# Performance work log

Measured on AMD Instinct MI355X. Metric: run time of the kernel, lower is better.

The kernel has to match this reference:

```python
import jax, jax.numpy as jnp
import numpy as np

K = 16  # number of neighbors (module init arg)

def setup_inputs() -> dict:
    key = jax.random.key(0)
    M, D, N = 65536, 16, 64
    x = jax.random.normal(key, (M, D), dtype=jnp.float32)
    # equal-length segments: each point set has M // N points
    segs = jnp.full((N,), M // N, dtype=jnp.int64)
    return {"x": x, "segs": segs}

def reference(x, segs):
    # Segmented kNN graph. Segments are equal-length (static shapes for jit),
    # so the per-segment pairwise distance + top-k becomes a batched op.
    B = segs.shape[0]
    M, D = x.shape
    L = M // B  # points per segment
    pts = x.reshape(B, L, D)
    # squared euclidean distances within each segment: (B, L, L)
    sq = jnp.sum(pts * pts, axis=-1)
    d2 = sq[:, :, None] + sq[:, None, :] - 2.0 * jnp.einsum('bld,bmd->blm', pts, pts)
    # k smallest distances per point (includes self, as in DGL's knn_graph)
    _, idx = jax.lax.top_k(-d2, K)  # idx: (B, L, K), local indices within segment
    offsets = (jnp.arange(B, dtype=idx.dtype) * L)[:, None, None]
    src = (idx + offsets).reshape(-1)                      # neighbor -> global node id
    dst = (jnp.arange(L, dtype=idx.dtype)[None, :, None] + offsets)  # (B, L, 1)
    dst = jnp.broadcast_to(dst, (B, L, K)).reshape(-1)
    # edges point from k-nearest neighbors (predecessors) to each node
    return src, dst
```

## Files before the change

kernel.cpp:

```cpp
#include <hip/hip_runtime.h>
#include <stdint.h>


#define L_SEG 1024
#define M_PTS 65536

typedef __fp16 fp16x2 __attribute__((ext_vector_type(2)));
typedef __fp16 fp16x4 __attribute__((ext_vector_type(4)));
typedef float  f32x4  __attribute__((ext_vector_type(4)));

__device__ __forceinline__ uint32_t umn(uint32_t a, uint32_t b) { return a < b ? a : b; }
__device__ __forceinline__ uint32_t umx(uint32_t a, uint32_t b) { return a > b ? a : b; }

#define CE(arr, i, p) { uint32_t lo = umn(arr[i], arr[p]); uint32_t hi = umx(arr[i], arr[p]); arr[i] = lo; arr[p] = hi; }

__device__ __forceinline__ void clean16(uint32_t* A) {
    #pragma unroll
    for (int j = 8; j > 0; j >>= 1) {
        #pragma unroll
        for (int i = 0; i < 16; ++i) {
            int p = i ^ j;
            if (p > i) CE(A, i, p);
        }
    }
}

__device__ __forceinline__ void sort16(uint32_t* B) {
    #pragma unroll
    for (int p = 1; p < 16; p <<= 1) {
        #pragma unroll
        for (int k = p; k >= 1; k >>= 1) {
            #pragma unroll
            for (int j = (k & (p - 1)); j + k < 16; j += 2 * k) {
                #pragma unroll
                for (int i = 0; i <= ((k - 1 < 15 - j - k) ? k - 1 : 15 - j - k); ++i) {
                    if ((i + j) / (2 * p) == (i + j + k) / (2 * p)) CE(B, i + j, i + j + k);
                }
            }
        }
    }
}

__device__ __forceinline__ void keep16(uint32_t* A, const uint32_t* S) {
    #pragma unroll
    for (int i = 0; i < 16; ++i) A[i] = umn(A[i], S[15 - i]);
    clean16(A);
}

__device__ __forceinline__ void mergeg(uint32_t* A) {
    #pragma unroll
    for (int m = 16; m <= 32; m <<= 1) {
        uint32_t P[16];
        #pragma unroll
        for (int i = 0; i < 16; ++i) P[i] = (uint32_t)__shfl_xor((int)A[15 - i], m, 64);
        #pragma unroll
        for (int i = 0; i < 16; ++i) A[i] = umn(A[i], P[i]);
        clean16(A);
    }
}

__device__ __forceinline__ uint32_t sel4(const uint32_t* A, int g, int v) {
    uint32_t t01 = (g & 1) ? A[4 + v]  : A[v];
    uint32_t t23 = (g & 1) ? A[12 + v] : A[8 + v];
    return (g & 2) ? t23 : t01;
}

__device__ __forceinline__ void batch16(const __fp16* ap, const float* sqp,
                                        fp16x4 bfrag, int it, int g, uint32_t* P) {
    #pragma unroll
    for (int t = 0; t < 16; ++t) {
        const int cb = it * 256 + t * 16;
        fp16x4 af = *(const fp16x4*)(ap + (size_t)cb * 16);
        f32x4  sq = *(const f32x4*)(sqp + cb);
        f32x4 acc = __builtin_amdgcn_mfma_f32_16x16x16f16(af, bfrag, sq, 0, 0, 0);
        float m = fminf(fminf(fminf(acc[0], acc[1]), acc[2]), acc[3]);
        P[t] = (__float_as_uint(m) & 0xFFFFFF00u) | (uint32_t)(it * 64 + t * 4) | (uint32_t)g;
    }
}

__global__ __launch_bounds__(1024, 1) void knn_v17_kernel(const float* __restrict__ x,
                                                          int* __restrict__ out) {
    __shared__ __attribute__((aligned(16))) __fp16 sc[L_SEG * 16];
    __shared__ __attribute__((aligned(16))) float  ssq[L_SEG];

    const int tid  = threadIdx.x;
    const int b    = blockIdx.x;
    const int seg  = b >> 2;
    const int qgrp = (b & 3) << 8;
    const float* xseg = x + (size_t)seg * (L_SEG * 16);
    const f32x4* gx4  = (const f32x4*)xseg;

    {
        fp16x4* scv = (fp16x4*)sc;
        const int widx = (tid & ~3) + ((tid & 3) ^ ((tid >> 4) & 3));
        #pragma unroll
        for (int i = 0; i < 4; ++i) {
            f32x4 v = gx4[tid + 1024 * i];
            union { fp16x2 h2[2]; fp16x4 h4; } u;
            u.h2[0] = __builtin_amdgcn_cvt_pkrtz(-2.0f * v[0], -2.0f * v[1]);
            u.h2[1] = __builtin_amdgcn_cvt_pkrtz(-2.0f * v[2], -2.0f * v[3]);
            scv[widx + 1024 * i] = u.h4;
            float p = v[0] * v[0];
            p = __builtin_fmaf(v[1], v[1], p);
            p = __builtin_fmaf(v[2], v[2], p);
            p = __builtin_fmaf(v[3], v[3], p);
            p += __shfl_xor(p, 1, 64);
            p += __shfl_xor(p, 2, 64);
            if ((tid & 3) == 0) ssq[(tid >> 2) + 256 * i] = p + 128.0f;
        }
    }
    __syncthreads();

    const int lane = tid & 63;
    const int w    = tid >> 6;
    const int g    = lane >> 4;
    const int col  = lane & 15;
    const int qrow = qgrp + w * 16 + col;
    const int gsw  = g ^ ((col >> 2) & 3);

    const fp16x4 mh = {(__fp16)-0.5f, (__fp16)-0.5f, (__fp16)-0.5f, (__fp16)-0.5f};
    fp16x4 bfrag;
    {
        fp16x4 raw = *(const fp16x4*)(sc + (size_t)qrow * 16 + gsw * 4);
        bfrag = raw * mh;
    }

    const __fp16* ap  = sc + (size_t)col * 16 + gsw * 4;
    const float*  sqp = ssq + g * 4;

    uint32_t P0[16], P1[16], P2[16], P3[16];
    batch16(ap, sqp, bfrag, 0, g, P0);
    batch16(ap, sqp, bfrag, 1, g, P1);
    batch16(ap, sqp, bfrag, 2, g, P2);
    batch16(ap, sqp, bfrag, 3, g, P3);
    sort16(P0);
    sort16(P1);
    sort16(P2);
    sort16(P3);
    keep16(P0, P1);
    keep16(P2, P3);
    keep16(P0, P2);
    uint32_t* A = P0;

    mergeg(A);

    uint32_t R[16];
    {
        const uint32_t c2a = (uint32_t)(col & 4);
        const uint32_t c2b = (uint32_t)(col & 8);
        const uint32_t v0  = (uint32_t)(col & 3);
        #pragma unroll
        for (int j = 0; j < 4; ++j) {
            const uint32_t t01 = c2a ? A[4*j + 1] : A[4*j + 0];
            const uint32_t t23 = c2a ? A[4*j + 3] : A[4*j + 2];
            const uint32_t awc = c2b ? t23 : t01;
            const uint32_t qid = awc & 255u;
            const uint32_t mrow = (qid << 2) | v0;
            const uint32_t msw = ((uint32_t)g ^ (qid & 3u)) << 2;
            fp16x4 af = *(const fp16x4*)(sc + (size_t)mrow * 16 + msw);
            const uint32_t u01 = (g & 1) ? A[4*j + 1] : A[4*j + 0];
            const uint32_t u23 = (g & 1) ? A[4*j + 3] : A[4*j + 2];
            const uint32_t awg = (g & 2) ? u23 : u01;
            const uint32_t ib  = (awg & 255u) << 2;
            f32x4 sq = *(const f32x4*)(ssq + (size_t)ib);
            f32x4 acc = __builtin_amdgcn_mfma_f32_16x16x16f16(af, bfrag, sq, 0, 0, 0);
            R[j*4 + 0] = (__float_as_uint(acc[0]) & 0xFFFFFC00u) | ib;
            R[j*4 + 1] = (__float_as_uint(acc[1]) & 0xFFFFFC00u) | (ib + 1u);
            R[j*4 + 2] = (__float_as_uint(acc[2]) & 0xFFFFFC00u) | (ib + 2u);
            R[j*4 + 3] = (__float_as_uint(acc[3]) & 0xFFFFFC00u) | (ib + 3u);
        }
    }
    sort16(R);
    mergeg(R);

    const int base = seg * L_SEG;
    const int q    = base + qrow;
    int4 sv;
    sv.x = base + (int)(sel4(R, g, 0) & 1023u);
    sv.y = base + (int)(sel4(R, g, 1) & 1023u);
    sv.z = base + (int)(sel4(R, g, 2) & 1023u);
    sv.w = base + (int)(sel4(R, g, 3) & 1023u);
    ((int4*)out)[(size_t)q * 4 + g] = sv;
    ((int4*)out)[(size_t)M_PTS * 4 + (size_t)q * 4 + g] = make_int4(q, q, q, q);
}

extern "C" void kernel_launch(void* const* d_in, const int* in_sizes, int n_in,
                              void* d_out, int out_size, void* d_ws, size_t ws_size,
                              hipStream_t stream) {
    const float* x = (const float*)d_in[0];
    int* out = (int*)d_out;
    (void)d_ws; (void)ws_size;
    knn_v17_kernel<<<dim3(256), dim3(1024), 0, stream>>>(x, out);
}
```

Before: 74.89 us.

## Pipeline segment staging into LDS with distance batches, starting at the block's own quarter

The kernel no longer stages the whole 1024-point segment into shared memory before computing. It first stages only the quarter that holds the block's own query rows. Each remaining quarter is fetched from global memory and written to LDS while the MFMA distance batch for an already-staged quarter runs. This is meant to hide global load latency behind compute, in exchange for three extra block-wide barriers and a batch order that now differs per block.

```diff
diff --git a/kernel.cpp b/kernel.cpp
--- a/kernel.cpp
+++ b/kernel.cpp
@@ -78,7 +78,23 @@
     }
 }
 
-__global__ __launch_bounds__(1024, 1) void knn_v17_kernel(const float* __restrict__ x,
+__device__ __forceinline__ void stage_store(__fp16* sc, float* ssq, int widx,
+                                            int tid, int j, f32x4 v) {
+    fp16x4* scv = (fp16x4*)sc;
+    union { fp16x2 h2[2]; fp16x4 h4; } u;
+    u.h2[0] = __builtin_amdgcn_cvt_pkrtz(-2.0f * v[0], -2.0f * v[1]);
+    u.h2[1] = __builtin_amdgcn_cvt_pkrtz(-2.0f * v[2], -2.0f * v[3]);
+    scv[widx + 1024 * j] = u.h4;
+    float p = v[0] * v[0];
+    p = __builtin_fmaf(v[1], v[1], p);
+    p = __builtin_fmaf(v[2], v[2], p);
+    p = __builtin_fmaf(v[3], v[3], p);
+    p += __shfl_xor(p, 1, 64);
+    p += __shfl_xor(p, 2, 64);
+    if ((tid & 3) == 0) ssq[(tid >> 2) + 256 * j] = p + 128.0f;
+}
+
+__global__ __launch_bounds__(1024, 1) void knn_v18_kernel(const float* __restrict__ x,
                                                           int* __restrict__ out) {
     __shared__ __attribute__((aligned(16))) __fp16 sc[L_SEG * 16];
     __shared__ __attribute__((aligned(16))) float  ssq[L_SEG];
@@ -86,29 +102,14 @@
     const int tid  = threadIdx.x;
     const int b    = blockIdx.x;
     const int seg  = b >> 2;
-    const int qgrp = (b & 3) << 8;
+    const int j0   = b & 3;
+    const int qgrp = j0 << 8;
     const float* xseg = x + (size_t)seg * (L_SEG * 16);
     const f32x4* gx4  = (const f32x4*)xseg;
 
-    {
-        fp16x4* scv = (fp16x4*)sc;
-        const int widx = (tid & ~3) + ((tid & 3) ^ ((tid >> 4) & 3));
-        #pragma unroll
-        for (int i = 0; i < 4; ++i) {
-            f32x4 v = gx4[tid + 1024 * i];
-            union { fp16x2 h2[2]; fp16x4 h4; } u;
-            u.h2[0] = __builtin_amdgcn_cvt_pkrtz(-2.0f * v[0], -2.0f * v[1]);
-            u.h2[1] = __builtin_amdgcn_cvt_pkrtz(-2.0f * v[2], -2.0f * v[3]);
-            scv[widx + 1024 * i] = u.h4;
-            float p = v[0] * v[0];
-            p = __builtin_fmaf(v[1], v[1], p);
-            p = __builtin_fmaf(v[2], v[2], p);
-            p = __builtin_fmaf(v[3], v[3], p);
-            p += __shfl_xor(p, 1, 64);
-            p += __shfl_xor(p, 2, 64);
-            if ((tid & 3) == 0) ssq[(tid >> 2) + 256 * i] = p + 128.0f;
-        }
-    }
+    const int widx = (tid & ~3) + ((tid & 3) ^ ((tid >> 4) & 3));
+
+    stage_store(sc, ssq, widx, tid, j0, gx4[tid + 1024 * j0]);
     __syncthreads();
 
     const int lane = tid & 63;
@@ -129,10 +130,26 @@
     const float*  sqp = ssq + g * 4;
 
     uint32_t P0[16], P1[16], P2[16], P3[16];
-    batch16(ap, sqp, bfrag, 0, g, P0);
-    batch16(ap, sqp, bfrag, 1, g, P1);
-    batch16(ap, sqp, bfrag, 2, g, P2);
-    batch16(ap, sqp, bfrag, 3, g, P3);
+    {
+        f32x4 vn = gx4[tid + 1024 * (j0 ^ 1)];
+        batch16(ap, sqp, bfrag, j0, g, P0);
+        stage_store(sc, ssq, widx, tid, j0 ^ 1, vn);
+        __syncthreads();
+    }
+    {
+        f32x4 vn = gx4[tid + 1024 * (j0 ^ 2)];
+        batch16(ap, sqp, bfrag, j0 ^ 1, g, P1);
+        stage_store(sc, ssq, widx, tid, j0 ^ 2, vn);
+        __syncthreads();
+    }
+    {
+        f32x4 vn = gx4[tid + 1024 * (j0 ^ 3)];
+        batch16(ap, sqp, bfrag, j0 ^ 2, g, P2);
+        stage_store(sc, ssq, widx, tid, j0 ^ 3, vn);
+        __syncthreads();
+    }
+    batch16(ap, sqp, bfrag, j0 ^ 3, g, P3);
+
     sort16(P0);
     sort16(P1);
     sort16(P2);
@@ -190,5 +207,5 @@
     const float* x = (const float*)d_in[0];
     int* out = (int*)d_out;
     (void)d_ws; (void)ws_size;
-    knn_v17_kernel<<<dim3(256), dim3(1024), 0, stream>>>(x, out);
-}
+    knn_v18_kernel<<<dim3(256), dim3(1024), 0, stream>>>(x, out);
+}
```

New measurement: 105.3 us. +40.7%, slower.
